# Kernel tuning notes

Hardware: AMD Instinct MI355X
Metric: run time of the kernel (lower is better)

Reference implementation:

```python
import jax, jax.numpy as jnp
import numpy as np

M, N, DIM, BATCH = 100, 100, 32, 128
GRID = M * N
ALPHA = 0.05
SIGMA = np.sqrt(GRID) / 2.0  # default sigma = sqrt(m*n)/2 = 50.0


def setup_inputs() -> dict:
    key = jax.random.key(0)
    k1, k2, k3 = jax.random.split(key, 3)
    x = jax.random.normal(k1, (BATCH, DIM), dtype=jnp.float32)
    centroids = jax.random.normal(k2, (GRID, DIM), dtype=jnp.float32)
    # grid locations [(i, j) for i in range(m) for j in range(n)]
    ii, jj = jnp.meshgrid(jnp.arange(M, dtype=jnp.int32), jnp.arange(N, dtype=jnp.int32), indexing='ij')
    locations = jnp.stack([ii.ravel(), jj.ravel()], axis=1)  # [GRID, 2]
    # precomputed non-periodic squared grid distances: [GRID, GRID]
    locf = locations.astype(jnp.float32)
    dr = locf[:, 0][:, None] - locf[:, 0][None, :]
    dc = locf[:, 1][:, None] - locf[:, 1][None, :]
    distance_mat = dr * dr + dc * dc
    learning_rate_op = jax.random.uniform(k3, (1,), dtype=jnp.float32) * 0.5 + 0.25
    return {"x": x, "centroids": centroids, "locations": locations,
            "distance_mat": distance_mat, "learning_rate_op": learning_rate_op}


def reference(x, centroids, locations, distance_mat, learning_rate_op):
    lr = learning_rate_op[0]
    # torch.cdist(x[:, None, :], centroids, p=2) -> [B, GRID]
    x2 = jnp.sum(x * x, axis=1, keepdims=True)            # [B, 1]
    c2 = jnp.sum(centroids * centroids, axis=1)           # [GRID]
    d2 = jnp.maximum(x2 + c2[None, :] - 2.0 * (x @ centroids.T), 0.0)
    dists = jnp.sqrt(d2)                                  # [B, GRID]
    mindist = jnp.min(dists, axis=-1)                     # [B]
    bmu_index = jnp.argmin(dists, axis=-1)                # [B]
    bmu_loc = locations[bmu_index]                        # [B, 2]
    alpha_op = ALPHA * lr
    sigma_op = SIGMA * lr
    # irregular gather of precomputed neighbourhood rows: [B, GRID]
    bmu_distance_squares = distance_mat[bmu_index]
    neighbourhood = jnp.exp(-bmu_distance_squares / (2.0 * sigma_op ** 2 + 1e-5))
    lrm = alpha_op * neighbourhood                        # [B, GRID]
    # delta = mean_b lrm[b,g] * (x[b,:] - centroids[g,:])  (no [B,GRID,DIM] temp)
    B = x.shape[0]
    delta = (jnp.einsum('bg,bd->gd', lrm, x) - jnp.sum(lrm, axis=0)[:, None] * centroids) / B
    new_weights = centroids + delta                       # [GRID, DIM]
    return bmu_loc, jnp.mean(mindist), new_weights
```

## Files before the change

kernel.cpp:

```cpp
#include <hip/hip_runtime.h>
#include <math.h>

#define BATCH 128
#define GRID_N 10000
#define DIM 32
#define MCOLS 100
#define NCHUNK 8
#define GCHUNK 1250

__global__ __launch_bounds__(256) void k1_bmu(const float* __restrict__ x,
                                              const float* __restrict__ c,
                                              float* __restrict__ pmin,
                                              int* __restrict__ pidx) {
    const int blk   = blockIdx.x;
    const int bg    = blk >> 3;
    const int chunk = blk & 7;
    const int b0    = bg * 4;
    const int t     = threadIdx.x;

    float xr[4][DIM];
#pragma unroll
    for (int i = 0; i < 4; ++i)
#pragma unroll
        for (int d = 0; d < DIM; ++d)
            xr[i][d] = x[(b0 + i) * DIM + d];

    const int gstart = chunk * GCHUNK;
    const int gend   = gstart + GCHUNK;

    float best[4] = {3.4e38f, 3.4e38f, 3.4e38f, 3.4e38f};
    int   idx[4]  = {0, 0, 0, 0};

    for (int g = gstart + t; g < gend; g += 256) {
        const float4* cr = (const float4*)(c + (size_t)g * DIM);
        float d2[4] = {0.f, 0.f, 0.f, 0.f};
#pragma unroll
        for (int k = 0; k < 8; ++k) {
            float4 cv = cr[k];
#pragma unroll
            for (int i = 0; i < 4; ++i) {
                float a;
                a = xr[i][4*k+0] - cv.x; d2[i] = fmaf(a, a, d2[i]);
                a = xr[i][4*k+1] - cv.y; d2[i] = fmaf(a, a, d2[i]);
                a = xr[i][4*k+2] - cv.z; d2[i] = fmaf(a, a, d2[i]);
                a = xr[i][4*k+3] - cv.w; d2[i] = fmaf(a, a, d2[i]);
            }
        }
#pragma unroll
        for (int i = 0; i < 4; ++i)
            if (d2[i] < best[i]) { best[i] = d2[i]; idx[i] = g; }
    }

#pragma unroll
    for (int m = 1; m < 64; m <<= 1) {
#pragma unroll
        for (int i = 0; i < 4; ++i) {
            float o  = __shfl_xor(best[i], m);
            int   oi = __shfl_xor(idx[i], m);
            if (o < best[i] || (o == best[i] && oi < idx[i])) { best[i] = o; idx[i] = oi; }
        }
    }

    __shared__ float sm[4][4];
    __shared__ int   si[4][4];
    const int wave = t >> 6;
    const int lane = t & 63;
    if (lane == 0) {
#pragma unroll
        for (int i = 0; i < 4; ++i) { sm[i][wave] = best[i]; si[i][wave] = idx[i]; }
    }
    __syncthreads();
    if (t < 4) {
        float bb = sm[t][0]; int bi = si[t][0];
#pragma unroll
        for (int w = 1; w < 4; ++w)
            if (sm[t][w] < bb || (sm[t][w] == bb && si[t][w] < bi)) { bb = sm[t][w]; bi = si[t][w]; }
        pmin[(b0 + t) * NCHUNK + chunk] = bb;
        pidx[(b0 + t) * NCHUNK + chunk] = bi;
    }
}

__global__ __launch_bounds__(256) void k3_update(const float* __restrict__ x,
                                                 const float* __restrict__ c,
                                                 const int* __restrict__ loc,
                                                 const float* __restrict__ pmin,
                                                 const int* __restrict__ pidx,
                                                 const float* __restrict__ lrp,
                                                 float* __restrict__ out) {
    __shared__ float bi_s[BATCH], bj_s[BATCH];
    __shared__ float red[4][64][33];
    __shared__ float partial[2];

    const int t = threadIdx.x;

    float msum = 0.f;
    if (t < BATCH) {
        float best = pmin[t * NCHUNK];
        int   bi   = pidx[t * NCHUNK];
#pragma unroll
        for (int k = 1; k < NCHUNK; ++k) {
            float v = pmin[t * NCHUNK + k];
            int   i = pidx[t * NCHUNK + k];
            if (v < best || (v == best && i < bi)) { best = v; bi = i; }
        }
        const float li = (float)loc[2 * bi];
        const float lj = (float)loc[2 * bi + 1];
        bi_s[t] = li;
        bj_s[t] = lj;
        if (blockIdx.x == 0) { out[2 * t] = li; out[2 * t + 1] = lj; }
        msum = sqrtf(fmaxf(best, 0.f));
    }
#pragma unroll
    for (int m = 1; m < 64; m <<= 1) msum += __shfl_xor(msum, m);
    if (t < BATCH && (t & 63) == 0) partial[t >> 6] = msum;
    __syncthreads();
    if (blockIdx.x == 0 && t == 0) out[256] = (partial[0] + partial[1]) * (1.0f / 128.0f);

    const float lr    = lrp[0];
    const float alpha = 0.05f * lr;
    const float sig   = 50.0f * lr;
    const float inv   = 1.0f / (2.0f * sig * sig + 1e-5f);

    const int gl = t & 63;
    const int ch = t >> 6;
    const int g  = blockIdx.x * 64 + gl;
    const float gi = (float)(g / MCOLS);
    const float gj = (float)(g % MCOLS);

    float acc[DIM];
#pragma unroll
    for (int d = 0; d < DIM; ++d) acc[d] = 0.f;
    float s0 = 0.f;

    const int bbase = ch * 32;
    for (int i = 0; i < 32; ++i) {
        const int bu = __builtin_amdgcn_readfirstlane(bbase + i);
        const float dr = gi - bi_s[bu];
        const float dc = gj - bj_s[bu];
        const float w  = alpha * __expf(-fmaf(dr, dr, dc * dc) * inv);
        s0 += w;
        const float4* xrp = (const float4*)(x + (size_t)bu * DIM);
#pragma unroll
        for (int k = 0; k < 8; ++k) {
            float4 xv = xrp[k];
            acc[4*k+0] = fmaf(w, xv.x, acc[4*k+0]);
            acc[4*k+1] = fmaf(w, xv.y, acc[4*k+1]);
            acc[4*k+2] = fmaf(w, xv.z, acc[4*k+2]);
            acc[4*k+3] = fmaf(w, xv.w, acc[4*k+3]);
        }
    }

#pragma unroll
    for (int d = 0; d < DIM; ++d) red[ch][gl][d] = acc[d];
    red[ch][gl][32] = s0;
    __syncthreads();

    const int gl2  = t >> 2;
    const int part = t & 3;
    const int g2   = blockIdx.x * 64 + gl2;
    if (g2 < GRID_N) {
        const float ssum = red[0][gl2][32] + red[1][gl2][32] +
                           red[2][gl2][32] + red[3][gl2][32];
#pragma unroll
        for (int k = 0; k < 8; ++k) {
            const int d = part * 8 + k;
            const float a  = red[0][gl2][d] + red[1][gl2][d] +
                             red[2][gl2][d] + red[3][gl2][d];
            const float cg = c[(size_t)g2 * DIM + d];
            out[257 + (size_t)g2 * DIM + d] = cg + (a - ssum * cg) * (1.0f / 128.0f);
        }
    }
}

extern "C" void kernel_launch(void* const* d_in, const int* in_sizes, int n_in,
                              void* d_out, int out_size, void* d_ws, size_t ws_size,
                              hipStream_t stream) {
    const float* x   = (const float*)d_in[0];
    const float* c   = (const float*)d_in[1];
    const int*   loc = (const int*)d_in[2];
    const float* lrp = (const float*)d_in[4];
    float* out = (float*)d_out;

    float* pmin = (float*)d_ws;
    int*   pidx = (int*)((char*)d_ws + 1024 * 4);

    hipLaunchKernelGGL(k1_bmu,    dim3(256), dim3(256), 0, stream, x, c, pmin, pidx);
    hipLaunchKernelGGL(k3_update, dim3(157), dim3(256), 0, stream, x, c, loc, pmin, pidx, lrp, out);
}
```

Measured before the change: 23.12 us.

## Fuse BMU search and update into one cooperative kernel with grid sync

Merges the two kernels into a single cooperative launch of 256 blocks, where a grid-wide sync separates the BMU partial-min phase from the neighbourhood-weighted centroid update. Partial results are exchanged through agent-scope atomic stores and loads. The aim is to drop the second kernel's launch cost and the gap between the two launches. In exchange it adds grid-sync overhead and requires all blocks to be co-resident, while blocks 157 and above sit idle after the sync.

New measurement: 53.95 us. 133% more time.

```diff
diff --git a/kernel.cpp b/kernel.cpp
--- a/kernel.cpp
+++ b/kernel.cpp
@@ -1,5 +1,8 @@
 #include <hip/hip_runtime.h>
+#include <hip/hip_cooperative_groups.h>
 #include <math.h>
+
+namespace cg = cooperative_groups;
 
 #define BATCH 128
 #define GRID_N 10000
@@ -7,114 +10,112 @@
 #define MCOLS 100
 #define NCHUNK 8
 #define GCHUNK 1250
+#define NBLK 256
 
-__global__ __launch_bounds__(256) void k1_bmu(const float* __restrict__ x,
-                                              const float* __restrict__ c,
-                                              float* __restrict__ pmin,
-                                              int* __restrict__ pidx) {
-    const int blk   = blockIdx.x;
-    const int bg    = blk >> 3;
-    const int chunk = blk & 7;
-    const int b0    = bg * 4;
-    const int t     = threadIdx.x;
-
-    float xr[4][DIM];
-#pragma unroll
-    for (int i = 0; i < 4; ++i)
-#pragma unroll
-        for (int d = 0; d < DIM; ++d)
-            xr[i][d] = x[(b0 + i) * DIM + d];
-
-    const int gstart = chunk * GCHUNK;
-    const int gend   = gstart + GCHUNK;
-
-    float best[4] = {3.4e38f, 3.4e38f, 3.4e38f, 3.4e38f};
-    int   idx[4]  = {0, 0, 0, 0};
-
-    for (int g = gstart + t; g < gend; g += 256) {
-        const float4* cr = (const float4*)(c + (size_t)g * DIM);
-        float d2[4] = {0.f, 0.f, 0.f, 0.f};
-#pragma unroll
-        for (int k = 0; k < 8; ++k) {
-            float4 cv = cr[k];
-#pragma unroll
-            for (int i = 0; i < 4; ++i) {
-                float a;
-                a = xr[i][4*k+0] - cv.x; d2[i] = fmaf(a, a, d2[i]);
-                a = xr[i][4*k+1] - cv.y; d2[i] = fmaf(a, a, d2[i]);
-                a = xr[i][4*k+2] - cv.z; d2[i] = fmaf(a, a, d2[i]);
-                a = xr[i][4*k+3] - cv.w; d2[i] = fmaf(a, a, d2[i]);
-            }
-        }
-#pragma unroll
-        for (int i = 0; i < 4; ++i)
-            if (d2[i] < best[i]) { best[i] = d2[i]; idx[i] = g; }
-    }
-
-#pragma unroll
-    for (int m = 1; m < 64; m <<= 1) {
-#pragma unroll
-        for (int i = 0; i < 4; ++i) {
-            float o  = __shfl_xor(best[i], m);
-            int   oi = __shfl_xor(idx[i], m);
-            if (o < best[i] || (o == best[i] && oi < idx[i])) { best[i] = o; idx[i] = oi; }
-        }
-    }
+__global__ __launch_bounds__(256) void som_fused(
+    const float* __restrict__ x, const float* __restrict__ c,
+    const int* __restrict__ loc, const float* __restrict__ lrp,
+    float* __restrict__ out, float* pmin, int* pidx)
+{
+    const int t   = threadIdx.x;
+    const int blk = blockIdx.x;
 
     __shared__ float sm[4][4];
     __shared__ int   si[4][4];
-    const int wave = t >> 6;
-    const int lane = t & 63;
-    if (lane == 0) {
-#pragma unroll
-        for (int i = 0; i < 4; ++i) { sm[i][wave] = best[i]; si[i][wave] = idx[i]; }
-    }
-    __syncthreads();
-    if (t < 4) {
-        float bb = sm[t][0]; int bi = si[t][0];
-#pragma unroll
-        for (int w = 1; w < 4; ++w)
-            if (sm[t][w] < bb || (sm[t][w] == bb && si[t][w] < bi)) { bb = sm[t][w]; bi = si[t][w]; }
-        pmin[(b0 + t) * NCHUNK + chunk] = bb;
-        pidx[(b0 + t) * NCHUNK + chunk] = bi;
-    }
-}
-
-__global__ __launch_bounds__(256) void k3_update(const float* __restrict__ x,
-                                                 const float* __restrict__ c,
-                                                 const int* __restrict__ loc,
-                                                 const float* __restrict__ pmin,
-                                                 const int* __restrict__ pidx,
-                                                 const float* __restrict__ lrp,
-                                                 float* __restrict__ out) {
     __shared__ float bi_s[BATCH], bj_s[BATCH];
     __shared__ float red[4][64][33];
     __shared__ float partial[2];
 
-    const int t = threadIdx.x;
+    {
+        const int bg    = blk >> 3;
+        const int chunk = blk & 7;
+        const int b0    = bg * 4;
+
+        float xr[4][DIM];
+#pragma unroll
+        for (int i = 0; i < 4; ++i)
+#pragma unroll
+            for (int d = 0; d < DIM; ++d)
+                xr[i][d] = x[(b0 + i) * DIM + d];
+
+        const int gstart = chunk * GCHUNK;
+        float best[4] = {3.4e38f, 3.4e38f, 3.4e38f, 3.4e38f};
+        int   idx[4]  = {0, 0, 0, 0};
+
+        for (int g = gstart + t; g < gstart + GCHUNK; g += 256) {
+            const float4* cr = (const float4*)(c + (size_t)g * DIM);
+            float d2[4] = {0.f, 0.f, 0.f, 0.f};
+#pragma unroll
+            for (int k = 0; k < 8; ++k) {
+                float4 cv = cr[k];
+#pragma unroll
+                for (int i = 0; i < 4; ++i) {
+                    float a;
+                    a = xr[i][4*k+0] - cv.x; d2[i] = fmaf(a, a, d2[i]);
+                    a = xr[i][4*k+1] - cv.y; d2[i] = fmaf(a, a, d2[i]);
+                    a = xr[i][4*k+2] - cv.z; d2[i] = fmaf(a, a, d2[i]);
+                    a = xr[i][4*k+3] - cv.w; d2[i] = fmaf(a, a, d2[i]);
+                }
+            }
+#pragma unroll
+            for (int i = 0; i < 4; ++i)
+                if (d2[i] < best[i]) { best[i] = d2[i]; idx[i] = g; }
+        }
+
+#pragma unroll
+        for (int m = 1; m < 64; m <<= 1) {
+#pragma unroll
+            for (int i = 0; i < 4; ++i) {
+                float o  = __shfl_xor(best[i], m);
+                int   oi = __shfl_xor(idx[i], m);
+                if (o < best[i] || (o == best[i] && oi < idx[i])) { best[i] = o; idx[i] = oi; }
+            }
+        }
+
+        const int wave = t >> 6, lane = t & 63;
+        if (lane == 0) {
+#pragma unroll
+            for (int i = 0; i < 4; ++i) { sm[i][wave] = best[i]; si[i][wave] = idx[i]; }
+        }
+        __syncthreads();
+        if (t < 4) {
+            float bb = sm[t][0]; int bi = si[t][0];
+#pragma unroll
+            for (int w = 1; w < 4; ++w)
+                if (sm[t][w] < bb || (sm[t][w] == bb && si[t][w] < bi)) { bb = sm[t][w]; bi = si[t][w]; }
+            __hip_atomic_store(&pmin[(b0 + t) * NCHUNK + chunk], bb,
+                               __ATOMIC_RELAXED, __HIP_MEMORY_SCOPE_AGENT);
+            __hip_atomic_store(&pidx[(b0 + t) * NCHUNK + chunk], bi,
+                               __ATOMIC_RELAXED, __HIP_MEMORY_SCOPE_AGENT);
+        }
+    }
+
+    cg::this_grid().sync();
+
+    if (blk >= 157) return;
 
     float msum = 0.f;
     if (t < BATCH) {
-        float best = pmin[t * NCHUNK];
-        int   bi   = pidx[t * NCHUNK];
+        float best = __hip_atomic_load(&pmin[t * NCHUNK], __ATOMIC_RELAXED, __HIP_MEMORY_SCOPE_AGENT);
+        int   bi   = __hip_atomic_load(&pidx[t * NCHUNK], __ATOMIC_RELAXED, __HIP_MEMORY_SCOPE_AGENT);
 #pragma unroll
         for (int k = 1; k < NCHUNK; ++k) {
-            float v = pmin[t * NCHUNK + k];
-            int   i = pidx[t * NCHUNK + k];
+            float v = __hip_atomic_load(&pmin[t * NCHUNK + k], __ATOMIC_RELAXED, __HIP_MEMORY_SCOPE_AGENT);
+            int   i = __hip_atomic_load(&pidx[t * NCHUNK + k], __ATOMIC_RELAXED, __HIP_MEMORY_SCOPE_AGENT);
             if (v < best || (v == best && i < bi)) { best = v; bi = i; }
         }
         const float li = (float)loc[2 * bi];
         const float lj = (float)loc[2 * bi + 1];
         bi_s[t] = li;
         bj_s[t] = lj;
-        if (blockIdx.x == 0) { out[2 * t] = li; out[2 * t + 1] = lj; }
+        if (blk == 0) { out[2 * t] = li; out[2 * t + 1] = lj; }
         msum = sqrtf(fmaxf(best, 0.f));
     }
 #pragma unroll
     for (int m = 1; m < 64; m <<= 1) msum += __shfl_xor(msum, m);
     if (t < BATCH && (t & 63) == 0) partial[t >> 6] = msum;
     __syncthreads();
-    if (blockIdx.x == 0 && t == 0) out[256] = (partial[0] + partial[1]) * (1.0f / 128.0f);
+    if (blk == 0 && t == 0) out[256] = (partial[0] + partial[1]) * (1.0f / 128.0f);
 
     const float lr    = lrp[0];
     const float alpha = 0.05f * lr;
@@ -123,7 +124,7 @@
 
     const int gl = t & 63;
     const int ch = t >> 6;
-    const int g  = blockIdx.x * 64 + gl;
+    const int g  = blk * 64 + gl;
     const float gi = (float)(g / MCOLS);
     const float gj = (float)(g % MCOLS);
 
@@ -157,7 +158,7 @@
 
     const int gl2  = t >> 2;
     const int part = t & 3;
-    const int g2   = blockIdx.x * 64 + gl2;
+    const int g2   = blk * 64 + gl2;
     if (g2 < GRID_N) {
         const float ssum = red[0][gl2][32] + red[1][gl2][32] +
                            red[2][gl2][32] + red[3][gl2][32];
@@ -184,6 +185,8 @@
     float* pmin = (float*)d_ws;
     int*   pidx = (int*)((char*)d_ws + 1024 * 4);
 
-    hipLaunchKernelGGL(k1_bmu,    dim3(256), dim3(256), 0, stream, x, c, pmin, pidx);
-    hipLaunchKernelGGL(k3_update, dim3(157), dim3(256), 0, stream, x, c, loc, pmin, pidx, lrp, out);
+    void* args[] = { (void*)&x, (void*)&c, (void*)&loc, (void*)&lrp,
+                     (void*)&out, (void*)&pmin, (void*)&pidx };
+    hipLaunchCooperativeKernel((const void*)som_fused, dim3(NBLK), dim3(256),
+                               args, 0, stream);
 }
```
